# Kernel optimization log

Hardware: AMD Instinct MI355X
Metric: run time of the kernel (lower is better)

Reference implementation:

```python
import jax, jax.numpy as jnp
import numpy as np

EPS = 1e-12  # tf.nn.l2_normalize epsilon

def _l2_normalize(x, axis):
    sq = jnp.sum(jnp.square(x), axis=axis, keepdims=True)
    return x * jax.lax.rsqrt(jnp.maximum(sq, EPS))

def setup_inputs() -> dict:
    key = jax.random.key(0)
    k1, k2 = jax.random.split(key)
    B, C, CLS = 8192, 512, 32000
    inputs = jax.random.normal(k1, (B, C), dtype=jnp.float32)
    # glorot_uniform for shape (C, CLS)
    limit = np.sqrt(6.0 / (C + CLS)).astype(np.float32)
    w = jax.random.uniform(k2, (C, CLS), dtype=jnp.float32, minval=-limit, maxval=limit)
    return {"inputs": inputs, "w": w}

def reference(inputs, w):
    # x: [B, C] l2-normalized over channel; w: [C, CLS] l2-normalized over channel.
    # The original broadcast-multiply-reduce over the channel axis == matmul.
    x = _l2_normalize(inputs, axis=-1)
    wn = _l2_normalize(w, axis=0)
    return jnp.einsum('bc,ck->bk', x, wn)  # [B, CLS] cosine similarities
```

## Files before the change

### kernel.cpp

```cpp
#include <hip/hip_runtime.h>
#include <hip/hip_bf16.h>
#include <stdint.h>

#define M_DIM 8192
#define K_DIM 512
#define N_DIM 32000

typedef short bf16x8 __attribute__((ext_vector_type(8)));
typedef float f32x4 __attribute__((ext_vector_type(4)));
typedef unsigned short u16;

__device__ __forceinline__ u16 f2bf(float f) {
  union { float f; uint32_t u; } v; v.f = f;
  uint32_t r = (v.u + 0x7fffu + ((v.u >> 16) & 1u)) >> 16;
  return (u16)r;
}

__global__ void k_xnorm(const float* __restrict__ x, u16* __restrict__ xn) {
  int row = (blockIdx.x * blockDim.x + threadIdx.x) >> 6;
  int lane = threadIdx.x & 63;
  const float4* rp = (const float4*)(x + (size_t)row * K_DIM);
  float4 a = rp[lane];
  float4 b = rp[lane + 64];
  float s = a.x*a.x + a.y*a.y + a.z*a.z + a.w*a.w
          + b.x*b.x + b.y*b.y + b.z*b.z + b.w*b.w;
#pragma unroll
  for (int off = 32; off > 0; off >>= 1) s += __shfl_xor(s, off, 64);
  float r = rsqrtf(fmaxf(s, 1e-12f));
  ushort4 o0 = make_ushort4(f2bf(a.x*r), f2bf(a.y*r), f2bf(a.z*r), f2bf(a.w*r));
  ushort4 o1 = make_ushort4(f2bf(b.x*r), f2bf(b.y*r), f2bf(b.z*r), f2bf(b.w*r));
  ushort4* dst = (ushort4*)(xn + (size_t)row * K_DIM);
  dst[lane] = o0;
  dst[lane + 64] = o1;
}

__global__ void k_wnorm(const float* __restrict__ w, float* __restrict__ cn) {
  int c = blockIdx.x * 256 + threadIdx.x;
  int rg = threadIdx.y;
  const float* p = w + (size_t)rg * 128 * N_DIM + c;
  float s = 0.f;
#pragma unroll 8
  for (int r = 0; r < 128; ++r) {
    float v = p[(size_t)r * N_DIM];
    s = fmaf(v, v, s);
  }
  __shared__ float red[4][256];
  red[rg][threadIdx.x] = s;
  __syncthreads();
  if (rg == 0) {
    float t = red[0][threadIdx.x] + red[1][threadIdx.x]
            + red[2][threadIdx.x] + red[3][threadIdx.x];
    cn[c] = rsqrtf(fmaxf(t, 1e-12f));
  }
}

__global__ void k_wtrans(const float* __restrict__ w, const float* __restrict__ cn,
                         u16* __restrict__ wT) {
  __shared__ u16 tile[64][68];
  int c0 = blockIdx.x * 64;
  int r0 = blockIdx.y * 64;
  int tc = threadIdx.x & 63;
  int tw = threadIdx.x >> 6;
  float scale = cn[c0 + tc];
#pragma unroll
  for (int i = 0; i < 16; ++i) {
    int r = i * 4 + tw;
    float v = w[(size_t)(r0 + r) * N_DIM + c0 + tc];
    tile[tc][r] = f2bf(v * scale);
  }
  __syncthreads();
  int cc = threadIdx.x >> 4;
  int rr = (threadIdx.x & 15) * 4;
#pragma unroll
  for (int i = 0; i < 4; ++i) {
    int c = cc + i * 16;
    ushort4 v = *(const ushort4*)&tile[c][rr];
    *(ushort4*)(wT + (size_t)(c0 + c) * K_DIM + r0 + rr) = v;
  }
}

__global__ __launch_bounds__(512, 2) void k_gemm(const u16* __restrict__ A,
                                                 const u16* __restrict__ Bt,
                                                 float* __restrict__ C) {
  __shared__ u16 sm[2][32768];
  constexpr int BOFF = 16384;

  int bid = blockIdx.x;
  bid = (bid & 7) * 500 + (bid >> 3);
  const int bm = bid / 125;
  const int bn = bid % 125;

  const int t = threadIdx.x;
  const int lane = t & 63;
  const int w = t >> 6;
  const int wr = w >> 2;
  const int wc = w & 3;
  const int la = lane & 15;
  const int lk = lane >> 4;
  const int rx = la & 7;
  const int s0 = ((0 + lk) ^ rx) * 8;
  const int s1 = ((4 + lk) ^ rx) * 8;

  f32x4 acc[8][4] = {};

  const int srow = t >> 3;
  const int sgl = ((t & 7) ^ (srow & 7)) * 8;
  const u16* ag = A  + (size_t)(bm * 256 + srow) * K_DIM + sgl;
  const u16* bg = Bt + (size_t)(bn * 256 + srow) * K_DIM + sgl;
  const int ldst = srow * 64 + (t & 7) * 8;

#pragma unroll
  for (int i = 0; i < 4; ++i)
    __builtin_amdgcn_global_load_lds(
        (const __attribute__((address_space(1))) void*)(ag + (size_t)i * 64 * K_DIM),
        (__attribute__((address_space(3))) void*)&sm[0][i * 4096 + ldst], 16, 0, 0);
#pragma unroll
  for (int i = 0; i < 4; ++i)
    __builtin_amdgcn_global_load_lds(
        (const __attribute__((address_space(1))) void*)(bg + (size_t)i * 64 * K_DIM),
        (__attribute__((address_space(3))) void*)&sm[0][BOFF + i * 4096 + ldst], 16, 0, 0);
  __syncthreads();

  const int arow0 = (wr * 128 + la) * 64;
  const int brow0 = (wc * 64 + la) * 64;

  for (int kt = 0; kt < 8; ++kt) {
    const int cur = kt & 1;
    const int nxt = cur ^ 1;
    const bool pf = (kt + 1) < 8;
    const int ko = (kt + 1) * 64;

    bf16x8 bf[4][2];

    {
#pragma unroll
      for (int n = 0; n < 4; ++n) {
        bf[n][0] = *(const bf16x8*)&sm[cur][BOFF + brow0 + n * 1024 + s0];
        bf[n][1] = *(const bf16x8*)&sm[cur][BOFF + brow0 + n * 1024 + s1];
      }
      bf16x8 af[2][2];
#pragma unroll
      for (int m = 0; m < 2; ++m) {
        af[m][0] = *(const bf16x8*)&sm[cur][arow0 + m * 1024 + s0];
        af[m][1] = *(const bf16x8*)&sm[cur][arow0 + m * 1024 + s1];
      }
      if (pf) {
#pragma unroll
        for (int i = 0; i < 4; ++i)
          __builtin_amdgcn_global_load_lds(
              (const __attribute__((address_space(1))) void*)(ag + (size_t)i * 64 * K_DIM + ko),
              (__attribute__((address_space(3))) void*)&sm[nxt][i * 4096 + ldst], 16, 0, 0);
      }
      __builtin_amdgcn_s_barrier();
      asm volatile("s_waitcnt lgkmcnt(0)" ::: "memory");
      __builtin_amdgcn_sched_barrier(0);
      __builtin_amdgcn_s_setprio(1);
#pragma unroll
      for (int m = 0; m < 2; ++m)
#pragma unroll
        for (int n = 0; n < 4; ++n) {
          acc[m][n] = __builtin_amdgcn_mfma_f32_16x16x32_bf16(af[m][0], bf[n][0], acc[m][n], 0, 0, 0);
          acc[m][n] = __builtin_amdgcn_mfma_f32_16x16x32_bf16(af[m][1], bf[n][1], acc[m][n], 0, 0, 0);
        }
      __builtin_amdgcn_s_setprio(0);
      __builtin_amdgcn_s_barrier();
    }

#pragma unroll
    for (int p = 1; p < 4; ++p) {
      bf16x8 af[2][2];
#pragma unroll
      for (int m = 0; m < 2; ++m) {
        af[m][0] = *(const bf16x8*)&sm[cur][arow0 + (p * 2 + m) * 1024 + s0];
        af[m][1] = *(const bf16x8*)&sm[cur][arow0 + (p * 2 + m) * 1024 + s1];
      }
      if (p == 1 && pf) {
#pragma unroll
        for (int i = 0; i < 4; ++i)
          __builtin_amdgcn_global_load_lds(
              (const __attribute__((address_space(1))) void*)(bg + (size_t)i * 64 * K_DIM + ko),
              (__attribute__((address_space(3))) void*)&sm[nxt][BOFF + i * 4096 + ldst], 16, 0, 0);
      }
      __builtin_amdgcn_s_barrier();
      asm volatile("s_waitcnt lgkmcnt(0)" ::: "memory");
      __builtin_amdgcn_sched_barrier(0);
      __builtin_amdgcn_s_setprio(1);
#pragma unroll
      for (int m = 0; m < 2; ++m)
#pragma unroll
        for (int n = 0; n < 4; ++n) {
          acc[p * 2 + m][n] = __builtin_amdgcn_mfma_f32_16x16x32_bf16(af[m][0], bf[n][0], acc[p * 2 + m][n], 0, 0, 0);
          acc[p * 2 + m][n] = __builtin_amdgcn_mfma_f32_16x16x32_bf16(af[m][1], bf[n][1], acc[p * 2 + m][n], 0, 0, 0);
        }
      __builtin_amdgcn_s_setprio(0);
      if (p < 3) __builtin_amdgcn_s_barrier();
    }

    __syncthreads();
  }

  const size_t crow0 = (size_t)bm * 256 + wr * 128 + lk * 4;
  const int ccol0 = bn * 256 + wc * 64 + la;
#pragma unroll
  for (int m = 0; m < 8; ++m)
#pragma unroll
    for (int j = 0; j < 4; ++j) {
      float* cp = C + (crow0 + m * 16 + j) * N_DIM + ccol0;
#pragma unroll
      for (int n = 0; n < 4; ++n) cp[n * 16] = acc[m][n][j];
    }
}

extern "C" void kernel_launch(void* const* d_in, const int* in_sizes, int n_in,
                              void* d_out, int out_size, void* d_ws, size_t ws_size,
                              hipStream_t stream) {
  const float* x = (const float*)d_in[0];
  const float* w = (const float*)d_in[1];
  float* out = (float*)d_out;

  char* ws = (char*)d_ws;
  float* cn = (float*)ws;
  u16* xn = (u16*)(ws + 131072);
  u16* wT = (u16*)(ws + 131072 + (size_t)M_DIM * K_DIM * 2);

  k_xnorm<<<M_DIM / 4, 256, 0, stream>>>(x, xn);
  k_wnorm<<<N_DIM / 256, dim3(256, 4), 0, stream>>>(w, cn);
  k_wtrans<<<dim3(N_DIM / 64, K_DIM / 64), 256, 0, stream>>>(w, cn, wT);
  k_gemm<<<(M_DIM / 256) * (N_DIM / 256), 512, 0, stream>>>(xn, wT, out);
}
```

Measured before the change: 409.4 us.

## Make GEMM persistent with contiguous tile ranges and cross-tile prefetch

The GEMM launch drops from one block per 256x256 tile (4000 blocks) to 256 persistent blocks. Each block walks a contiguous range of 15 or 16 tiles in row-major order, so consecutive tiles share the A panel. The first K slice of the next tile is prefetched into LDS during the last K step of the current one, which hides tile start-up latency. Output stores now use nontemporal hints. The risks are a sequential epilogue inside each block that cannot overlap other blocks' compute, load imbalance between 15- and 16-tile blocks, and the loss of the previous interleaved block ordering, which may reduce L2 reuse of B.

```diff
diff --git a/kernel.cpp b/kernel.cpp
--- a/kernel.cpp
+++ b/kernel.cpp
@@ -5,6 +5,10 @@
 #define M_DIM 8192
 #define K_DIM 512
 #define N_DIM 32000
+#define NTILES 4000
+#define NBLK 256
+#define TPB_Q 15
+#define TPB_R 160
 
 typedef short bf16x8 __attribute__((ext_vector_type(8)));
 typedef float f32x4 __attribute__((ext_vector_type(4)));
@@ -85,14 +89,13 @@
   __shared__ u16 sm[2][32768];
   constexpr int BOFF = 16384;
 
-  int bid = blockIdx.x;
-  bid = (bid & 7) * 500 + (bid >> 3);
-  const int bm = bid / 125;
-  const int bn = bid % 125;
-
-  const int t = threadIdx.x;
-  const int lane = t & 63;
-  const int w = t >> 6;
+  const int b = blockIdx.x;
+  const int cnt = TPB_Q + (b < TPB_R ? 1 : 0);
+  int t = b * TPB_Q + (b < TPB_R ? b : TPB_R);
+
+  const int tid = threadIdx.x;
+  const int lane = tid & 63;
+  const int w = tid >> 6;
   const int wr = w >> 2;
   const int wc = w & 3;
   const int la = lane & 15;
@@ -101,13 +104,18 @@
   const int s0 = ((0 + lk) ^ rx) * 8;
   const int s1 = ((4 + lk) ^ rx) * 8;
 
-  f32x4 acc[8][4] = {};
-
-  const int srow = t >> 3;
-  const int sgl = ((t & 7) ^ (srow & 7)) * 8;
+  const int srow = tid >> 3;
+  const int sgl = ((tid & 7) ^ (srow & 7)) * 8;
+  const int ldst = srow * 64 + (tid & 7) * 8;
+  const int arow0 = (wr * 128 + la) * 64;
+  const int brow0 = (wc * 64 + la) * 64;
+
+  int bm = t / 125;
+  int bn = t - bm * 125;
   const u16* ag = A  + (size_t)(bm * 256 + srow) * K_DIM + sgl;
   const u16* bg = Bt + (size_t)(bn * 256 + srow) * K_DIM + sgl;
-  const int ldst = srow * 64 + (t & 7) * 8;
+
+  f32x4 acc[8][4] = {};
 
 #pragma unroll
   for (int i = 0; i < 4; ++i)
@@ -121,94 +129,110 @@
         (__attribute__((address_space(3))) void*)&sm[0][BOFF + i * 4096 + ldst], 16, 0, 0);
   __syncthreads();
 
-  const int arow0 = (wr * 128 + la) * 64;
-  const int brow0 = (wc * 64 + la) * 64;
-
-  for (int kt = 0; kt < 8; ++kt) {
-    const int cur = kt & 1;
-    const int nxt = cur ^ 1;
-    const bool pf = (kt + 1) < 8;
-    const int ko = (kt + 1) * 64;
-
-    bf16x8 bf[4][2];
+  for (int ti = 0; ti < cnt; ++ti) {
+    int bn1 = bn + 1, bm1 = bm;
+    if (bn1 == 125) { bn1 = 0; bm1 = bm + 1; }
+    const u16* agn = A  + (size_t)(bm1 * 256 + srow) * K_DIM + sgl;
+    const u16* bgn = Bt + (size_t)(bn1 * 256 + srow) * K_DIM + sgl;
+    const bool last_tile = (ti + 1 == cnt);
+
+    for (int kt = 0; kt < 8; ++kt) {
+      const int cur = kt & 1;
+      const int nxt = cur ^ 1;
+      const bool pf = (kt < 7) || !last_tile;
+      const u16* agk = (kt < 7) ? (ag + (kt + 1) * 64) : agn;
+      const u16* bgk = (kt < 7) ? (bg + (kt + 1) * 64) : bgn;
+
+      bf16x8 bf[4][2];
+
+      {
+#pragma unroll
+        for (int n = 0; n < 4; ++n) {
+          bf[n][0] = *(const bf16x8*)&sm[cur][BOFF + brow0 + n * 1024 + s0];
+          bf[n][1] = *(const bf16x8*)&sm[cur][BOFF + brow0 + n * 1024 + s1];
+        }
+        bf16x8 af[2][2];
+#pragma unroll
+        for (int m = 0; m < 2; ++m) {
+          af[m][0] = *(const bf16x8*)&sm[cur][arow0 + m * 1024 + s0];
+          af[m][1] = *(const bf16x8*)&sm[cur][arow0 + m * 1024 + s1];
+        }
+        if (pf) {
+#pragma unroll
+          for (int i = 0; i < 4; ++i)
+            __builtin_amdgcn_global_load_lds(
+                (const __attribute__((address_space(1))) void*)(agk + (size_t)i * 64 * K_DIM),
+                (__attribute__((address_space(3))) void*)&sm[nxt][i * 4096 + ldst], 16, 0, 0);
+        }
+        __builtin_amdgcn_s_barrier();
+        asm volatile("s_waitcnt lgkmcnt(0)" ::: "memory");
+        __builtin_amdgcn_sched_barrier(0);
+        __builtin_amdgcn_s_setprio(1);
+#pragma unroll
+        for (int m = 0; m < 2; ++m)
+#pragma unroll
+          for (int n = 0; n < 4; ++n) {
+            acc[m][n] = __builtin_amdgcn_mfma_f32_16x16x32_bf16(af[m][0], bf[n][0], acc[m][n], 0, 0, 0);
+            acc[m][n] = __builtin_amdgcn_mfma_f32_16x16x32_bf16(af[m][1], bf[n][1], acc[m][n], 0, 0, 0);
+          }
+        __builtin_amdgcn_s_setprio(0);
+        __builtin_amdgcn_s_barrier();
+      }
+
+#pragma unroll
+      for (int p = 1; p < 4; ++p) {
+        bf16x8 af[2][2];
+#pragma unroll
+        for (int m = 0; m < 2; ++m) {
+          af[m][0] = *(const bf16x8*)&sm[cur][arow0 + (p * 2 + m) * 1024 + s0];
+          af[m][1] = *(const bf16x8*)&sm[cur][arow0 + (p * 2 + m) * 1024 + s1];
+        }
+        if (p == 1 && pf) {
+#pragma unroll
+          for (int i = 0; i < 4; ++i)
+            __builtin_amdgcn_global_load_lds(
+                (const __attribute__((address_space(1))) void*)(bgk + (size_t)i * 64 * K_DIM),
+                (__attribute__((address_space(3))) void*)&sm[nxt][BOFF + i * 4096 + ldst], 16, 0, 0);
+        }
+        __builtin_amdgcn_s_barrier();
+        asm volatile("s_waitcnt lgkmcnt(0)" ::: "memory");
+        __builtin_amdgcn_sched_barrier(0);
+        __builtin_amdgcn_s_setprio(1);
+#pragma unroll
+        for (int m = 0; m < 2; ++m)
+#pragma unroll
+          for (int n = 0; n < 4; ++n) {
+            acc[p * 2 + m][n] = __builtin_amdgcn_mfma_f32_16x16x32_bf16(af[m][0], bf[n][0], acc[p * 2 + m][n], 0, 0, 0);
+            acc[p * 2 + m][n] = __builtin_amdgcn_mfma_f32_16x16x32_bf16(af[m][1], bf[n][1], acc[p * 2 + m][n], 0, 0, 0);
+          }
+        __builtin_amdgcn_s_setprio(0);
+        if (p < 3) __builtin_amdgcn_s_barrier();
+      }
+
+      __syncthreads();
+    }
 
     {
-#pragma unroll
-      for (int n = 0; n < 4; ++n) {
-        bf[n][0] = *(const bf16x8*)&sm[cur][BOFF + brow0 + n * 1024 + s0];
-        bf[n][1] = *(const bf16x8*)&sm[cur][BOFF + brow0 + n * 1024 + s1];
-      }
-      bf16x8 af[2][2];
-#pragma unroll
-      for (int m = 0; m < 2; ++m) {
-        af[m][0] = *(const bf16x8*)&sm[cur][arow0 + m * 1024 + s0];
-        af[m][1] = *(const bf16x8*)&sm[cur][arow0 + m * 1024 + s1];
-      }
-      if (pf) {
-#pragma unroll
-        for (int i = 0; i < 4; ++i)
-          __builtin_amdgcn_global_load_lds(
-              (const __attribute__((address_space(1))) void*)(ag + (size_t)i * 64 * K_DIM + ko),
-              (__attribute__((address_space(3))) void*)&sm[nxt][i * 4096 + ldst], 16, 0, 0);
-      }
-      __builtin_amdgcn_s_barrier();
-      asm volatile("s_waitcnt lgkmcnt(0)" ::: "memory");
-      __builtin_amdgcn_sched_barrier(0);
-      __builtin_amdgcn_s_setprio(1);
-#pragma unroll
-      for (int m = 0; m < 2; ++m)
-#pragma unroll
-        for (int n = 0; n < 4; ++n) {
-          acc[m][n] = __builtin_amdgcn_mfma_f32_16x16x32_bf16(af[m][0], bf[n][0], acc[m][n], 0, 0, 0);
-          acc[m][n] = __builtin_amdgcn_mfma_f32_16x16x32_bf16(af[m][1], bf[n][1], acc[m][n], 0, 0, 0);
-        }
-      __builtin_amdgcn_s_setprio(0);
-      __builtin_amdgcn_s_barrier();
+      const size_t crow0 = (size_t)bm * 256 + wr * 128 + lk * 4;
+      const int ccol0 = bn * 256 + wc * 64 + la;
+#pragma unroll
+      for (int m = 0; m < 8; ++m)
+#pragma unroll
+        for (int j = 0; j < 4; ++j) {
+          float* cp = C + (crow0 + m * 16 + j) * N_DIM + ccol0;
+#pragma unroll
+          for (int n = 0; n < 4; ++n)
+            __builtin_nontemporal_store(acc[m][n][j], cp + n * 16);
+        }
+#pragma unroll
+      for (int m = 0; m < 8; ++m)
+#pragma unroll
+        for (int n = 0; n < 4; ++n)
+          acc[m][n] = (f32x4){0.f, 0.f, 0.f, 0.f};
     }
 
-#pragma unroll
-    for (int p = 1; p < 4; ++p) {
-      bf16x8 af[2][2];
-#pragma unroll
-      for (int m = 0; m < 2; ++m) {
-        af[m][0] = *(const bf16x8*)&sm[cur][arow0 + (p * 2 + m) * 1024 + s0];
-        af[m][1] = *(const bf16x8*)&sm[cur][arow0 + (p * 2 + m) * 1024 + s1];
-      }
-      if (p == 1 && pf) {
-#pragma unroll
-        for (int i = 0; i < 4; ++i)
-          __builtin_amdgcn_global_load_lds(
-              (const __attribute__((address_space(1))) void*)(bg + (size_t)i * 64 * K_DIM + ko),
-              (__attribute__((address_space(3))) void*)&sm[nxt][BOFF + i * 4096 + ldst], 16, 0, 0);
-      }
-      __builtin_amdgcn_s_barrier();
-      asm volatile("s_waitcnt lgkmcnt(0)" ::: "memory");
-      __builtin_amdgcn_sched_barrier(0);
-      __builtin_amdgcn_s_setprio(1);
-#pragma unroll
-      for (int m = 0; m < 2; ++m)
-#pragma unroll
-        for (int n = 0; n < 4; ++n) {
-          acc[p * 2 + m][n] = __builtin_amdgcn_mfma_f32_16x16x32_bf16(af[m][0], bf[n][0], acc[p * 2 + m][n], 0, 0, 0);
-          acc[p * 2 + m][n] = __builtin_amdgcn_mfma_f32_16x16x32_bf16(af[m][1], bf[n][1], acc[p * 2 + m][n], 0, 0, 0);
-        }
-      __builtin_amdgcn_s_setprio(0);
-      if (p < 3) __builtin_amdgcn_s_barrier();
-    }
-
-    __syncthreads();
-  }
-
-  const size_t crow0 = (size_t)bm * 256 + wr * 128 + lk * 4;
-  const int ccol0 = bn * 256 + wc * 64 + la;
-#pragma unroll
-  for (int m = 0; m < 8; ++m)
-#pragma unroll
-    for (int j = 0; j < 4; ++j) {
-      float* cp = C + (crow0 + m * 16 + j) * N_DIM + ccol0;
-#pragma unroll
-      for (int n = 0; n < 4; ++n) cp[n * 16] = acc[m][n][j];
-    }
+    bm = bm1; bn = bn1; ag = agn; bg = bgn;
+  }
 }
 
 extern "C" void kernel_launch(void* const* d_in, const int* in_sizes, int n_in,
@@ -226,5 +250,5 @@
   k_xnorm<<<M_DIM / 4, 256, 0, stream>>>(x, xn);
   k_wnorm<<<N_DIM / 256, dim3(256, 4), 0, stream>>>(w, cn);
   k_wtrans<<<dim3(N_DIM / 64, K_DIM / 64), 256, 0, stream>>>(w, cn, wT);
-  k_gemm<<<(M_DIM / 256) * (N_DIM / 256), 512, 0, stream>>>(xn, wT, out);
-}
+  k_gemm<<<NBLK, 512, 0, stream>>>(xn, wT, out);
+}
```

Result: slower. 514.3 us, median of 3 (+25.6%).
